# Performance work log

Measured on AMD Instinct MI355X. Metric: run time of the kernel, lower is better.

Reference implementation:

```python
import jax, jax.numpy as jnp
import numpy as np

B, T, D = 4, 2048, 2048
H = 16
HO = D // H  # head_out = 128


def setup_inputs() -> dict:
    key = jax.random.key(0)
    ks = jax.random.split(key, 6)
    x = jax.random.normal(ks[0], (B, T, D), dtype=jnp.float32)
    scale = 0.02
    Wq = jax.random.normal(ks[1], (D, D), dtype=jnp.float32) * scale
    Wk = jax.random.normal(ks[2], (D, D), dtype=jnp.float32) * scale
    Wv = jax.random.normal(ks[3], (D, D), dtype=jnp.float32) * scale
    Wp = jax.random.normal(ks[4], (D, D), dtype=jnp.float32) * scale
    bp = jnp.zeros((D,), dtype=jnp.float32)
    return {"x": x, "Wq": Wq, "Wk": Wk, "Wv": Wv, "Wp": Wp, "bp": bp}


def reference(x, Wq, Wk, Wv, Wp, bp):
    b, t, _ = x.shape
    # QKV projections (weights stored [d_in, d_out])
    q = x @ Wq
    k = x @ Wk
    v = x @ Wv
    split = lambda a: a.reshape(b, t, H, HO).transpose(0, 2, 1, 3)  # [b,H,T,ho]
    qh, kh, vh = split(q), split(k), split(v)
    # Feature attention: contract over tokens -> [b,H,ho,ho]
    scores = jnp.einsum('bhtf,bhtg->bhfg', qh, kh) / jnp.sqrt(jnp.float32(HO))
    weights = jax.nn.softmax(scores, axis=-1)  # dropout p=0.0 (identity)
    # feature_alibi: [1/T, 1/(T-1), ..., 1], broadcast over batch/head/feature
    feat_alibi = (1.0 / jnp.arange(t, 0, -1, dtype=jnp.float32)).reshape(1, 1, t, 1)
    vh = vh + feat_alibi
    # (weights @ v^T)^T : ctx[b,h,t,f] = sum_g weights[b,h,f,g] * v[b,h,t,g]
    ctx = jnp.einsum('bhfg,bhtg->bhtf', weights, vh)
    ctx = ctx.transpose(0, 2, 1, 3).reshape(b, t, H * HO)  # [b,T,d_out]
    return ctx @ Wp + bp
```

## Files before the change

kernel.cpp:

```cpp
#include <hip/hip_runtime.h>
#include <hip/hip_bf16.h>


#define Tt 2048
#define Dd 2048
#define Mm 8192

typedef __attribute__((ext_vector_type(4))) float f32x4;
typedef __attribute__((ext_vector_type(8))) short s16x8;
static_assert(sizeof(s16x8) == 16, "frag size");

typedef const __attribute__((address_space(1))) void* gptr_t;
typedef __attribute__((address_space(3))) void* lptr_t;

__device__ __forceinline__ float bf2f(ushort u) {
    union { unsigned int i; float f; } c; c.i = ((unsigned int)u) << 16; return c.f;
}
__device__ __forceinline__ ushort f2bf(float f) {
    union { float f; unsigned int i; } c; c.f = f;
    return (ushort)((c.i + 0x7FFFu + ((c.i >> 16) & 1u)) >> 16);
}
__device__ __forceinline__ void gload16(const void* g, void* l) {
    __builtin_amdgcn_global_load_lds((gptr_t)g, (lptr_t)l, 16, 0, 0);
}
__device__ __forceinline__ s16x8 ldfrag(const char* p) { return *(const s16x8*)p; }

#define MFMA_BF16(d, a, b) \
    asm("v_mfma_f32_16x16x32_bf16 %0, %1, %2, %0" : "+v"(d) : "v"(a), "v"(b))


__global__ __launch_bounds__(256) void convx_kernel(const float* __restrict__ x,
                                                    ushort* __restrict__ xb) {
    const int idx = blockIdx.x * 256 + threadIdx.x;
    const int stride = gridDim.x * 256;
    for (int i = idx; i < Mm * Dd / 4; i += stride) {
        const float4 v = *(const float4*)(x + (size_t)i * 4);
        ushort4 o; o.x = f2bf(v.x); o.y = f2bf(v.y); o.z = f2bf(v.z); o.w = f2bf(v.w);
        *(ushort4*)(xb + (size_t)i * 4) = o;
    }
}

__global__ __launch_bounds__(256) void transw_kernel(const float* __restrict__ W0,
        const float* __restrict__ W1, const float* __restrict__ W2,
        const float* __restrict__ W3, ushort* __restrict__ Wt) {
    __shared__ float tile[64][65];
    const int z = blockIdx.z;
    const float* W = (z == 0) ? W0 : (z == 1) ? W1 : (z == 2) ? W2 : W3;
    ushort* dst = Wt + (size_t)z * ((size_t)Dd * Dd);
    const int n0 = blockIdx.x * 64, k0 = blockIdx.y * 64;
    const int r4 = threadIdx.x >> 6, c = threadIdx.x & 63;
#pragma unroll
    for (int i = 0; i < 16; i++) {
        const int row = i * 4 + r4;
        tile[row][c] = W[(size_t)(k0 + row) * Dd + n0 + c];
    }
    __syncthreads();
#pragma unroll
    for (int i = 0; i < 16; i++) {
        const int row = i * 4 + r4;
        dst[(size_t)(n0 + row) * Dd + k0 + c] = f2bf(tile[c][row]);
    }
}


__device__ __forceinline__ void stage_half(char* ldsRegion, const ushort* gRegion,
                                           int ld, int half, int tid) {
#pragma unroll
    for (int j = 0; j < 2; j++) {
        const int Pb = half * 16384 + j * 8192 + (tid >> 6) * 1024;
        const int P = Pb + (tid & 63) * 16;
        const int row = P >> 7;
        const int colb = (P ^ ((row & 7) << 4)) & 127;
        gload16(gRegion + (size_t)row * ld + (colb >> 1), ldsRegion + Pb);
    }
}

template <int MODE>
__global__ __launch_bounds__(512, 2) void gemm256_kernel(
        const ushort* __restrict__ A, const ushort* __restrict__ Bt,
        void* __restrict__ Cv, const float* __restrict__ bias,
        int Kdim, int lda, int ldb, int ldc,
        size_t bstride, size_t cstride) {
    extern __shared__ char lds[];

    const int tid = threadIdx.x;
    const int lane = tid & 63;
    const int w = tid >> 6;
    const int wr = w >> 2, wc = w & 3;
    const int fr = lane & 15, fq = lane >> 4;

    const int bid = blockIdx.x;
    const int wg = (bid & 7) * 32 + (bid >> 3);
    const int m0 = (wg >> 3) * 256;
    const int n0 = (wg & 7) * 256;

    const ushort* Ag = A + (size_t)m0 * lda;
    const ushort* Bg = Bt + (size_t)blockIdx.z * bstride + (size_t)n0 * ldb;
    const int NT = Kdim >> 6;

    const int aoff = wr * 16384 + fr * 128;
    const int boff = wc * 8192 + fr * 128;
    const int xo = (fr & 7) << 4;
    const int cp0 = (fq * 16) ^ xo;
    const int cp1 = (64 + fq * 16) ^ xo;

    char* buf0 = lds;
    char* buf1 = lds + 65536;
    const char* Ab0 = buf0 + aoff;
    const char* Bb0 = buf0 + 32768 + boff;
    const char* Ab1 = buf1 + aoff;
    const char* Bb1 = buf1 + 32768 + boff;

    f32x4 acc[8][4];
#pragma unroll
    for (int i = 0; i < 8; i++)
#pragma unroll
        for (int j = 0; j < 4; j++) acc[i][j] = {0.f, 0.f, 0.f, 0.f};

    s16x8 afX[4][2], afY[4][2], bf01[2][2], bf23[2][2];

    {
        stage_half(buf0,         Ag, lda, 0, tid);
        stage_half(buf0,         Ag, lda, 1, tid);
        stage_half(buf0 + 32768, Bg, ldb, 0, tid);
        stage_half(buf0 + 32768, Bg, ldb, 1, tid);
        stage_half(buf1,         Ag + 64, lda, 0, tid);
        stage_half(buf1,         Ag + 64, lda, 1, tid);
        stage_half(buf1 + 32768, Bg + 64, ldb, 0, tid);
        stage_half(buf1 + 32768, Bg + 64, ldb, 1, tid);
        __builtin_amdgcn_sched_barrier(0);
        asm volatile("s_waitcnt vmcnt(8)" ::: "memory");
        __builtin_amdgcn_s_barrier();
    }

    const int NI = NT >> 1;
    for (int j = 0; j < NI; ++j) {
        const int e = 2 * j;
        const bool sAo = (j > 0);
        const bool sE2 = (e + 2 < NT);
        const bool sO2 = (e + 3 < NT);
        const ushort* AgO  = Ag + (size_t)(e + 1) * 64;
        const ushort* AgE2 = Ag + (size_t)(e + 2) * 64;
        const ushort* BgE2 = Bg + (size_t)(e + 2) * 64;
        const ushort* BgO2 = Bg + (size_t)(e + 3) * 64;

#pragma unroll
        for (int m = 0; m < 4; m++) {
            afX[m][0] = ldfrag(Ab0 + m * 2048 + cp0);
            afX[m][1] = ldfrag(Ab0 + m * 2048 + cp1);
        }
#pragma unroll
        for (int n = 0; n < 2; n++) {
            bf01[n][0] = ldfrag(Bb0 + n * 2048 + cp0);
            bf01[n][1] = ldfrag(Bb0 + n * 2048 + cp1);
        }
        if (sAo) stage_half(buf1, AgO, lda, 0, tid);
        __builtin_amdgcn_sched_barrier(0);
        asm volatile("s_waitcnt lgkmcnt(8)" ::: "memory");
        __builtin_amdgcn_s_barrier();
        asm volatile("s_waitcnt lgkmcnt(0)" ::: "memory");
        __builtin_amdgcn_sched_barrier(0);
        __builtin_amdgcn_s_setprio(1);
#pragma unroll
        for (int k = 0; k < 2; k++)
#pragma unroll
            for (int m = 0; m < 4; m++)
#pragma unroll
                for (int n = 0; n < 2; n++) MFMA_BF16(acc[m][n], afX[m][k], bf01[n][k]);
        __builtin_amdgcn_s_setprio(0);
        __builtin_amdgcn_s_barrier();

#pragma unroll
        for (int n = 0; n < 2; n++) {
            bf23[n][0] = ldfrag(Bb0 + (n + 2) * 2048 + cp0);
            bf23[n][1] = ldfrag(Bb0 + (n + 2) * 2048 + cp1);
        }
        if (sAo) stage_half(buf1, AgO, lda, 1, tid);
        __builtin_amdgcn_sched_barrier(0);
        __builtin_amdgcn_s_barrier();
        asm volatile("s_waitcnt lgkmcnt(0)" ::: "memory");
        __builtin_amdgcn_sched_barrier(0);
        __builtin_amdgcn_s_setprio(1);
#pragma unroll
        for (int k = 0; k < 2; k++)
#pragma unroll
            for (int m = 0; m < 4; m++)
#pragma unroll
                for (int n = 0; n < 2; n++) MFMA_BF16(acc[m][n + 2], afX[m][k], bf23[n][k]);
        __builtin_amdgcn_s_setprio(0);
        __builtin_amdgcn_s_barrier();

#pragma unroll
        for (int m = 0; m < 4; m++) {
            afY[m][0] = ldfrag(Ab0 + (m + 4) * 2048 + cp0);
            afY[m][1] = ldfrag(Ab0 + (m + 4) * 2048 + cp1);
        }
        if (sE2) stage_half(buf0 + 32768, BgE2, ldb, 0, tid);
        __builtin_amdgcn_sched_barrier(0);
        __builtin_amdgcn_s_barrier();
        asm volatile("s_waitcnt lgkmcnt(0)" ::: "memory");
        __builtin_amdgcn_sched_barrier(0);
        __builtin_amdgcn_s_setprio(1);
#pragma unroll
        for (int k = 0; k < 2; k++)
#pragma unroll
            for (int m = 0; m < 4; m++)
#pragma unroll
                for (int n = 0; n < 2; n++) MFMA_BF16(acc[m + 4][n], afY[m][k], bf01[n][k]);
        __builtin_amdgcn_s_setprio(0);
        __builtin_amdgcn_s_barrier();

        if (sE2) stage_half(buf0 + 32768, BgE2, ldb, 1, tid);
        __builtin_amdgcn_sched_barrier(0);
        __builtin_amdgcn_s_setprio(1);
#pragma unroll
        for (int k = 0; k < 2; k++)
#pragma unroll
            for (int m = 0; m < 4; m++)
#pragma unroll
                for (int n = 0; n < 2; n++) MFMA_BF16(acc[m + 4][n + 2], afY[m][k], bf23[n][k]);
        __builtin_amdgcn_s_setprio(0);
        __builtin_amdgcn_sched_barrier(0);
        if (sE2) asm volatile("s_waitcnt vmcnt(4)" ::: "memory");
        else     asm volatile("s_waitcnt vmcnt(0)" ::: "memory");
        __builtin_amdgcn_s_barrier();

#pragma unroll
        for (int m = 0; m < 4; m++) {
            afX[m][0] = ldfrag(Ab1 + m * 2048 + cp0);
            afX[m][1] = ldfrag(Ab1 + m * 2048 + cp1);
        }
#pragma unroll
        for (int n = 0; n < 2; n++) {
            bf01[n][0] = ldfrag(Bb1 + n * 2048 + cp0);
            bf01[n][1] = ldfrag(Bb1 + n * 2048 + cp1);
        }
        if (sE2) stage_half(buf0, AgE2, lda, 0, tid);
        __builtin_amdgcn_sched_barrier(0);
        asm volatile("s_waitcnt lgkmcnt(8)" ::: "memory");
        __builtin_amdgcn_s_barrier();
        asm volatile("s_waitcnt lgkmcnt(0)" ::: "memory");
        __builtin_amdgcn_sched_barrier(0);
        __builtin_amdgcn_s_setprio(1);
#pragma unroll
        for (int k = 0; k < 2; k++)
#pragma unroll
            for (int m = 0; m < 4; m++)
#pragma unroll
                for (int n = 0; n < 2; n++) MFMA_BF16(acc[m][n], afX[m][k], bf01[n][k]);
        __builtin_amdgcn_s_setprio(0);
        __builtin_amdgcn_s_barrier();

#pragma unroll
        for (int n = 0; n < 2; n++) {
            bf23[n][0] = ldfrag(Bb1 + (n + 2) * 2048 + cp0);
            bf23[n][1] = ldfrag(Bb1 + (n + 2) * 2048 + cp1);
        }
        if (sE2) stage_half(buf0, AgE2, lda, 1, tid);
        __builtin_amdgcn_sched_barrier(0);
        __builtin_amdgcn_s_barrier();
        asm volatile("s_waitcnt lgkmcnt(0)" ::: "memory");
        __builtin_amdgcn_sched_barrier(0);
        __builtin_amdgcn_s_setprio(1);
#pragma unroll
        for (int k = 0; k < 2; k++)
#pragma unroll
            for (int m = 0; m < 4; m++)
#pragma unroll
                for (int n = 0; n < 2; n++) MFMA_BF16(acc[m][n + 2], afX[m][k], bf23[n][k]);
        __builtin_amdgcn_s_setprio(0);
        __builtin_amdgcn_s_barrier();

#pragma unroll
        for (int m = 0; m < 4; m++) {
            afY[m][0] = ldfrag(Ab1 + (m + 4) * 2048 + cp0);
            afY[m][1] = ldfrag(Ab1 + (m + 4) * 2048 + cp1);
        }
        if (sO2) stage_half(buf1 + 32768, BgO2, ldb, 0, tid);
        __builtin_amdgcn_sched_barrier(0);
        __builtin_amdgcn_s_barrier();
        asm volatile("s_waitcnt lgkmcnt(0)" ::: "memory");
        __builtin_amdgcn_sched_barrier(0);
        __builtin_amdgcn_s_setprio(1);
#pragma unroll
        for (int k = 0; k < 2; k++)
#pragma unroll
            for (int m = 0; m < 4; m++)
#pragma unroll
                for (int n = 0; n < 2; n++) MFMA_BF16(acc[m + 4][n], afY[m][k], bf01[n][k]);
        __builtin_amdgcn_s_setprio(0);
        __builtin_amdgcn_s_barrier();

        if (sO2) stage_half(buf1 + 32768, BgO2, ldb, 1, tid);
        __builtin_amdgcn_sched_barrier(0);
        __builtin_amdgcn_s_setprio(1);
#pragma unroll
        for (int k = 0; k < 2; k++)
#pragma unroll
            for (int m = 0; m < 4; m++)
#pragma unroll
                for (int n = 0; n < 2; n++) MFMA_BF16(acc[m + 4][n + 2], afY[m][k], bf23[n][k]);
        __builtin_amdgcn_s_setprio(0);
        __builtin_amdgcn_sched_barrier(0);
        if (sO2) asm volatile("s_waitcnt vmcnt(4)" ::: "memory");
        else     asm volatile("s_waitcnt vmcnt(0)" ::: "memory");
        __builtin_amdgcn_s_barrier();
    }

    asm volatile("s_nop 7\ns_nop 7\ns_nop 7");

    if (MODE == 2) {
        float* C = (float*)Cv;
#pragma unroll
        for (int mi = 0; mi < 8; mi++)
#pragma unroll
            for (int ni = 0; ni < 4; ni++)
#pragma unroll
                for (int r = 0; r < 4; r++) {
                    const int row = m0 + wr * 128 + mi * 16 + fq * 4 + r;
                    const int col = n0 + wc * 64 + ni * 16 + fr;
                    C[(size_t)row * ldc + col] = acc[mi][ni][r] + bias[col];
                }
    } else {
        ushort* C = (ushort*)Cv + (size_t)blockIdx.z * cstride;
#pragma unroll
        for (int mi = 0; mi < 8; mi++)
#pragma unroll
            for (int ni = 0; ni < 4; ni++)
#pragma unroll
                for (int r = 0; r < 4; r++) {
                    const int row = m0 + wr * 128 + mi * 16 + fq * 4 + r;
                    const int col = n0 + wc * 64 + ni * 16 + fr;
                    C[(size_t)row * ldc + col] = f2bf(acc[mi][ni][r]);
                }
    }
}


template <int MODE>
__global__ __launch_bounds__(256, 2) void gemm_kernel(
        const ushort* __restrict__ A, const ushort* __restrict__ Bt,
        void* __restrict__ Cv, const float* __restrict__ bias,
        int Kdim, int lda, int ldb, int ldc) {
    __shared__ ushort lsA[128 * 32];
    __shared__ ushort lsB[128 * 32];

    const int tid = threadIdx.x;
    const int w = tid >> 6, lane = tid & 63;
    const int m0 = blockIdx.y * 128;
    const int n0 = blockIdx.x * 128;

    const ushort* Ab = A;
    const ushort* Bb = Bt;
    size_t coff = 0;
    if (MODE == 1) {
        const int z = blockIdx.z, b = z >> 4, h = z & 15;
        const size_t ao = (size_t)b * ((size_t)Tt * Dd) + (size_t)h * 128;
        Ab += ao; Bb += (size_t)z * (128 * 128); coff = ao;
    }

    const int sr = lane >> 2;
    const int sc = (lane & 3) * 8;
    const int c0 = w, c1 = w + 4;
    const int rA0 = c0 * 16 + sr, rA1 = c1 * 16 + sr;

    const int fr = lane & 15, fq = lane >> 4;
    const int wr = (w >> 1) * 64, wc = (w & 1) * 64;

    f32x4 acc[4][4];
#pragma unroll
    for (int i = 0; i < 4; i++)
#pragma unroll
        for (int j = 0; j < 4; j++) acc[i][j] = {0.f, 0.f, 0.f, 0.f};

    for (int kt = 0; kt < Kdim; kt += 32) {
        gload16(Ab + (size_t)(m0 + rA0) * lda + kt + sc, lsA + c0 * 512);
        gload16(Ab + (size_t)(m0 + rA1) * lda + kt + sc, lsA + c1 * 512);
        gload16(Bb + (size_t)(n0 + rA0) * ldb + kt + sc, lsB + c0 * 512);
        gload16(Bb + (size_t)(n0 + rA1) * ldb + kt + sc, lsB + c1 * 512);
        __syncthreads();

        s16x8 afrag[4], bfrag[4];
#pragma unroll
        for (int i = 0; i < 4; i++)
            afrag[i] = *(const s16x8*)(lsA + (wr + i * 16 + fr) * 32 + fq * 8);
#pragma unroll
        for (int j = 0; j < 4; j++)
            bfrag[j] = *(const s16x8*)(lsB + (wc + j * 16 + fr) * 32 + fq * 8);
#pragma unroll
        for (int i = 0; i < 4; i++)
#pragma unroll
            for (int j = 0; j < 4; j++)
                MFMA_BF16(acc[i][j], afrag[i], bfrag[j]);
        __syncthreads();
    }

    asm volatile("s_nop 7\ns_nop 7\ns_nop 7");

    {
        ushort* C = (ushort*)Cv + coff;
#pragma unroll
        for (int i = 0; i < 4; i++)
#pragma unroll
            for (int j = 0; j < 4; j++)
#pragma unroll
                for (int r = 0; r < 4; r++) {
                    const int row = m0 + wr + i * 16 + fq * 4 + r;
                    const int col = n0 + wc + j * 16 + fr;
                    float val = acc[i][j][r];
                    if (MODE == 1) val += 1.0f / (float)(Tt - row);
                    C[(size_t)row * ldc + col] = f2bf(val);
                }
    }
}


__global__ __launch_bounds__(256) void scores_kernel(const ushort* __restrict__ q,
        const ushort* __restrict__ k, float* __restrict__ part) {
    __shared__ float lsQ[32][128];
    __shared__ float lsK[32][128];
    const int tid = threadIdx.x;
    const int s = blockIdx.x, bh = blockIdx.y;
    const int b = bh >> 4, h = bh & 15;
    const size_t base = (size_t)b * ((size_t)Tt * Dd) + (size_t)h * 128;
    const ushort* qb = q + base;
    const ushort* kb = k + base;
    const int ty = tid >> 4, tx = tid & 15;
    const int f0 = ty * 8, g0 = tx * 8;

    float acc[8][8];
#pragma unroll
    for (int i = 0; i < 8; i++)
#pragma unroll
        for (int j = 0; j < 8; j++) acc[i][j] = 0.f;

    for (int ch = 0; ch < 16; ch++) {
        const int t0 = s * 512 + ch * 32;
#pragma unroll
        for (int ii = 0; ii < 4; ii++) {
            const int e = ii * 1024 + tid * 4;
            const int r = e >> 7, cc = e & 127;
            const size_t ga = (size_t)(t0 + r) * Dd + cc;
            const ushort4 v4 = *(const ushort4*)(qb + ga);
            f32x4 qf = {bf2f(v4.x), bf2f(v4.y), bf2f(v4.z), bf2f(v4.w)};
            *(f32x4*)&lsQ[r][cc] = qf;
            const ushort4 w4 = *(const ushort4*)(kb + ga);
            f32x4 kf = {bf2f(w4.x), bf2f(w4.y), bf2f(w4.z), bf2f(w4.w)};
            *(f32x4*)&lsK[r][cc] = kf;
        }
        __syncthreads();
#pragma unroll 4
        for (int tl = 0; tl < 32; tl++) {
            float qv[8], kv[8];
            *(f32x4*)&qv[0] = *(const f32x4*)&lsQ[tl][f0];
            *(f32x4*)&qv[4] = *(const f32x4*)&lsQ[tl][f0 + 4];
            *(f32x4*)&kv[0] = *(const f32x4*)&lsK[tl][g0];
            *(f32x4*)&kv[4] = *(const f32x4*)&lsK[tl][g0 + 4];
#pragma unroll
            for (int i = 0; i < 8; i++)
#pragma unroll
                for (int j = 0; j < 8; j++)
                    acc[i][j] = fmaf(qv[i], kv[j], acc[i][j]);
        }
        __syncthreads();
    }
    float* pb = part + ((size_t)s * 64 + bh) * 16384;
#pragma unroll
    for (int i = 0; i < 8; i++) {
        f32x4 o0 = {acc[i][0], acc[i][1], acc[i][2], acc[i][3]};
        f32x4 o1 = {acc[i][4], acc[i][5], acc[i][6], acc[i][7]};
        *(f32x4*)&pb[(f0 + i) * 128 + g0] = o0;
        *(f32x4*)&pb[(f0 + i) * 128 + g0 + 4] = o1;
    }
}


__global__ __launch_bounds__(256) void softmax_kernel(const float* __restrict__ part,
                                                      ushort* __restrict__ wts) {
    const int tid = threadIdx.x;
    const int wv = tid >> 6, lane = tid & 63;
    const int row = blockIdx.x * 4 + wv;
    const float* p = part + (size_t)row * 128 + lane * 2;
    float v0 = 0.f, v1 = 0.f;
#pragma unroll
    for (int s = 0; s < 4; s++) {
        const float2 t = *(const float2*)(p + (size_t)s * 1048576);
        v0 += t.x; v1 += t.y;
    }
    const float sc = 0.088388347648318447f;
    v0 *= sc; v1 *= sc;
    float m = fmaxf(v0, v1);
#pragma unroll
    for (int off = 32; off > 0; off >>= 1) m = fmaxf(m, __shfl_xor(m, off));
    const float e0 = __expf(v0 - m), e1 = __expf(v1 - m);
    float smv = e0 + e1;
#pragma unroll
    for (int off = 32; off > 0; off >>= 1) smv += __shfl_xor(smv, off);
    const float inv = 1.0f / smv;
    ushort2 o; o.x = f2bf(e0 * inv); o.y = f2bf(e1 * inv);
    *(ushort2*)(wts + (size_t)row * 128 + lane * 2) = o;
}


extern "C" void kernel_launch(void* const* d_in, const int* in_sizes, int n_in,
                              void* d_out, int out_size, void* d_ws, size_t ws_size,
                              hipStream_t stream) {
    const float* x  = (const float*)d_in[0];
    const float* Wq = (const float*)d_in[1];
    const float* Wk = (const float*)d_in[2];
    const float* Wv = (const float*)d_in[3];
    const float* Wp = (const float*)d_in[4];
    const float* bp = (const float*)d_in[5];
    float* out = (float*)d_out;
    char* ws = (char*)d_ws;

    ushort* xb   = (ushort*)(ws);
    ushort* Wt   = (ushort*)(ws + (33ull << 20));
    ushort* q    = (ushort*)(ws + (65ull << 20));
    ushort* k    = (ushort*)(ws + (97ull << 20));
    ushort* v    = (ushort*)(ws + (129ull << 20));
    float*  part = (float*) (ws + (161ull << 20));
    ushort* wts  = (ushort*)(ws + (193ull << 20));
    ushort* ctx  = xb;

    const size_t WSZ = (size_t)Dd * Dd;
    const size_t QSTRIDE = (32ull << 20) / 2;

    static_cast<void>(hipFuncSetAttribute((const void*)gemm256_kernel<0>,
        hipFuncAttributeMaxDynamicSharedMemorySize, 131072));
    static_cast<void>(hipFuncSetAttribute((const void*)gemm256_kernel<2>,
        hipFuncAttributeMaxDynamicSharedMemorySize, 131072));

    convx_kernel<<<2048, 256, 0, stream>>>(x, xb);
    transw_kernel<<<dim3(32, 32, 4), 256, 0, stream>>>(Wq, Wk, Wv, Wp, Wt);

    gemm256_kernel<0><<<dim3(256, 1, 3), 512, 131072, stream>>>(
        xb, Wt, q, nullptr, 2048, 2048, 2048, 2048, WSZ, QSTRIDE);

    scores_kernel<<<dim3(4, 64), 256, 0, stream>>>(q, k, part);
    softmax_kernel<<<2048, 256, 0, stream>>>(part, wts);

    gemm_kernel<1><<<dim3(1, 16, 64), 256, 0, stream>>>(v, wts, ctx, nullptr, 128, 2048, 128, 2048);

    gemm256_kernel<2><<<dim3(256, 1, 1), 512, 131072, stream>>>(
        ctx, Wt + 3 * WSZ, out, bp, 2048, 2048, 2048, 2048, 0, 0);
}
```

Measured before the change: 376.8 us.

## Compute attention scores via per-batch Gram matrix X^T X instead of Q/K projections

Rewrites the scores as Wq_h^T (X^T X) Wk_h. It builds a bf16 transpose of x, forms a per-batch Gram matrix G = X^T X, multiplies by Wk, then runs a small MFMA GEMM (new mode 3) to produce split-K score partials. This replaces both the Q/K projection GEMMs and the scalar-FP32 scores kernel. Total GEMM FLOPs stay roughly the same, but the slow non-MFMA scores stage goes away. In exchange, the large-magnitude Gram and intermediate products are rounded to bf16, which can cost accuracy. It also switches MFMA from inline asm to the builtin and drops the trailing s_nop padding.

Measured after the change: 337.3 us. 1.12x faster.

```diff
diff --git a/kernel.cpp b/kernel.cpp
--- a/kernel.cpp
+++ b/kernel.cpp
@@ -26,17 +26,29 @@
 __device__ __forceinline__ s16x8 ldfrag(const char* p) { return *(const s16x8*)p; }
 
 #define MFMA_BF16(d, a, b) \
-    asm("v_mfma_f32_16x16x32_bf16 %0, %1, %2, %0" : "+v"(d) : "v"(a), "v"(b))
-
-
-__global__ __launch_bounds__(256) void convx_kernel(const float* __restrict__ x,
-                                                    ushort* __restrict__ xb) {
-    const int idx = blockIdx.x * 256 + threadIdx.x;
-    const int stride = gridDim.x * 256;
-    for (int i = idx; i < Mm * Dd / 4; i += stride) {
-        const float4 v = *(const float4*)(x + (size_t)i * 4);
-        ushort4 o; o.x = f2bf(v.x); o.y = f2bf(v.y); o.z = f2bf(v.z); o.w = f2bf(v.w);
-        *(ushort4*)(xb + (size_t)i * 4) = o;
+    d = __builtin_amdgcn_mfma_f32_16x16x32_bf16((a), (b), (d), 0, 0, 0)
+
+
+__global__ __launch_bounds__(256) void convxT_kernel(const float* __restrict__ x,
+        ushort* __restrict__ xb, ushort* __restrict__ xT) {
+    __shared__ float tile[64][65];
+    const int b = blockIdx.z;
+    const int t0 = blockIdx.y * 64, d0 = blockIdx.x * 64;
+    const int r4 = threadIdx.x >> 6, c = threadIdx.x & 63;
+#pragma unroll
+    for (int i = 0; i < 16; i++) {
+        const int row = i * 4 + r4;
+        const size_t g = ((size_t)b * Tt + t0 + row) * Dd + d0 + c;
+        const float val = x[g];
+        xb[g] = f2bf(val);
+        tile[row][c] = val;
+    }
+    __syncthreads();
+#pragma unroll
+    for (int i = 0; i < 16; i++) {
+        const int row = i * 4 + r4;
+        xT[(size_t)b * ((size_t)Dd * Tt) + (size_t)(d0 + row) * Tt + t0 + c] =
+            f2bf(tile[c][row]);
     }
 }
 
@@ -80,7 +92,7 @@
         const ushort* __restrict__ A, const ushort* __restrict__ Bt,
         void* __restrict__ Cv, const float* __restrict__ bias,
         int Kdim, int lda, int ldb, int ldc,
-        size_t bstride, size_t cstride) {
+        size_t astride, size_t bstride, size_t cstride) {
     extern __shared__ char lds[];
 
     const int tid = threadIdx.x;
@@ -90,11 +102,12 @@
     const int fr = lane & 15, fq = lane >> 4;
 
     const int bid = blockIdx.x;
-    const int wg = (bid & 7) * 32 + (bid >> 3);
+    const int cpx = (int)gridDim.x >> 3;
+    const int wg = (bid & 7) * cpx + (bid >> 3);
     const int m0 = (wg >> 3) * 256;
     const int n0 = (wg & 7) * 256;
 
-    const ushort* Ag = A + (size_t)m0 * lda;
+    const ushort* Ag = A + (size_t)blockIdx.z * astride + (size_t)m0 * lda;
     const ushort* Bg = Bt + (size_t)blockIdx.z * bstride + (size_t)n0 * ldb;
     const int NT = Kdim >> 6;
 
@@ -307,8 +320,6 @@
         __builtin_amdgcn_s_barrier();
     }
 
-    asm volatile("s_nop 7\ns_nop 7\ns_nop 7");
-
     if (MODE == 2) {
         float* C = (float*)Cv;
 #pragma unroll
@@ -358,6 +369,13 @@
         const size_t ao = (size_t)b * ((size_t)Tt * Dd) + (size_t)h * 128;
         Ab += ao; Bb += (size_t)z * (128 * 128); coff = ao;
     }
+    if (MODE == 3) {
+        const int z = blockIdx.z, s = z >> 6, bh = z & 63;
+        const int b = bh >> 4, h = bh & 15;
+        Ab += (size_t)h * 128 * Dd + (size_t)s * 512;
+        Bb += (size_t)b * ((size_t)Dd * Dd) + (size_t)h * 128 * Dd + (size_t)s * 512;
+        coff = (size_t)s * (64 * 16384) + (size_t)bh * 16384;
+    }
 
     const int sr = lane >> 2;
     const int sc = (lane & 3) * 8;
@@ -395,9 +413,19 @@
         __syncthreads();
     }
 
-    asm volatile("s_nop 7\ns_nop 7\ns_nop 7");
-
-    {
+    if (MODE == 3) {
+        float* C = (float*)Cv + coff;
+#pragma unroll
+        for (int i = 0; i < 4; i++)
+#pragma unroll
+            for (int j = 0; j < 4; j++)
+#pragma unroll
+                for (int r = 0; r < 4; r++) {
+                    const int row = m0 + wr + i * 16 + fq * 4 + r;
+                    const int col = n0 + wc + j * 16 + fr;
+                    C[(size_t)row * ldc + col] = acc[i][j][r];
+                }
+    } else {
         ushort* C = (ushort*)Cv + coff;
 #pragma unroll
         for (int i = 0; i < 4; i++)
@@ -411,66 +439,6 @@
                     if (MODE == 1) val += 1.0f / (float)(Tt - row);
                     C[(size_t)row * ldc + col] = f2bf(val);
                 }
-    }
-}
-
-
-__global__ __launch_bounds__(256) void scores_kernel(const ushort* __restrict__ q,
-        const ushort* __restrict__ k, float* __restrict__ part) {
-    __shared__ float lsQ[32][128];
-    __shared__ float lsK[32][128];
-    const int tid = threadIdx.x;
-    const int s = blockIdx.x, bh = blockIdx.y;
-    const int b = bh >> 4, h = bh & 15;
-    const size_t base = (size_t)b * ((size_t)Tt * Dd) + (size_t)h * 128;
-    const ushort* qb = q + base;
-    const ushort* kb = k + base;
-    const int ty = tid >> 4, tx = tid & 15;
-    const int f0 = ty * 8, g0 = tx * 8;
-
-    float acc[8][8];
-#pragma unroll
-    for (int i = 0; i < 8; i++)
-#pragma unroll
-        for (int j = 0; j < 8; j++) acc[i][j] = 0.f;
-
-    for (int ch = 0; ch < 16; ch++) {
-        const int t0 = s * 512 + ch * 32;
-#pragma unroll
-        for (int ii = 0; ii < 4; ii++) {
-            const int e = ii * 1024 + tid * 4;
-            const int r = e >> 7, cc = e & 127;
-            const size_t ga = (size_t)(t0 + r) * Dd + cc;
-            const ushort4 v4 = *(const ushort4*)(qb + ga);
-            f32x4 qf = {bf2f(v4.x), bf2f(v4.y), bf2f(v4.z), bf2f(v4.w)};
-            *(f32x4*)&lsQ[r][cc] = qf;
-            const ushort4 w4 = *(const ushort4*)(kb + ga);
-            f32x4 kf = {bf2f(w4.x), bf2f(w4.y), bf2f(w4.z), bf2f(w4.w)};
-            *(f32x4*)&lsK[r][cc] = kf;
-        }
-        __syncthreads();
-#pragma unroll 4
-        for (int tl = 0; tl < 32; tl++) {
-            float qv[8], kv[8];
-            *(f32x4*)&qv[0] = *(const f32x4*)&lsQ[tl][f0];
-            *(f32x4*)&qv[4] = *(const f32x4*)&lsQ[tl][f0 + 4];
-            *(f32x4*)&kv[0] = *(const f32x4*)&lsK[tl][g0];
-            *(f32x4*)&kv[4] = *(const f32x4*)&lsK[tl][g0 + 4];
-#pragma unroll
-            for (int i = 0; i < 8; i++)
-#pragma unroll
-                for (int j = 0; j < 8; j++)
-                    acc[i][j] = fmaf(qv[i], kv[j], acc[i][j]);
-        }
-        __syncthreads();
-    }
-    float* pb = part + ((size_t)s * 64 + bh) * 16384;
-#pragma unroll
-    for (int i = 0; i < 8; i++) {
-        f32x4 o0 = {acc[i][0], acc[i][1], acc[i][2], acc[i][3]};
-        f32x4 o1 = {acc[i][4], acc[i][5], acc[i][6], acc[i][7]};
-        *(f32x4*)&pb[(f0 + i) * 128 + g0] = o0;
-        *(f32x4*)&pb[(f0 + i) * 128 + g0 + 4] = o1;
     }
 }
 
@@ -514,34 +482,43 @@
     float* out = (float*)d_out;
     char* ws = (char*)d_ws;
 
-    ushort* xb   = (ushort*)(ws);
-    ushort* Wt   = (ushort*)(ws + (33ull << 20));
-    ushort* q    = (ushort*)(ws + (65ull << 20));
-    ushort* k    = (ushort*)(ws + (97ull << 20));
-    ushort* v    = (ushort*)(ws + (129ull << 20));
-    float*  part = (float*) (ws + (161ull << 20));
-    ushort* wts  = (ushort*)(ws + (193ull << 20));
-    ushort* ctx  = xb;
+    ushort* xb  = (ushort*)(ws);
+    ushort* xT  = (ushort*)(ws + (32ull << 20));
+    ushort* Wt  = (ushort*)(ws + (64ull << 20));
+    ushort* G   = (ushort*)(ws + (96ull << 20));
+    ushort* Hb  = (ushort*)(ws + (128ull << 20));
+    ushort* v   = (ushort*)(ws + (160ull << 20));
+    float*  part = (float*)(ws + (96ull << 20));
+    ushort* wts = (ushort*)(ws + (112ull << 20));
+    ushort* ctx = xT;
 
     const size_t WSZ = (size_t)Dd * Dd;
-    const size_t QSTRIDE = (32ull << 20) / 2;
 
     static_cast<void>(hipFuncSetAttribute((const void*)gemm256_kernel<0>,
         hipFuncAttributeMaxDynamicSharedMemorySize, 131072));
     static_cast<void>(hipFuncSetAttribute((const void*)gemm256_kernel<2>,
         hipFuncAttributeMaxDynamicSharedMemorySize, 131072));
 
-    convx_kernel<<<2048, 256, 0, stream>>>(x, xb);
+    convxT_kernel<<<dim3(32, 32, 4), 256, 0, stream>>>(x, xb, xT);
     transw_kernel<<<dim3(32, 32, 4), 256, 0, stream>>>(Wq, Wk, Wv, Wp, Wt);
 
-    gemm256_kernel<0><<<dim3(256, 1, 3), 512, 131072, stream>>>(
-        xb, Wt, q, nullptr, 2048, 2048, 2048, 2048, WSZ, QSTRIDE);
-
-    scores_kernel<<<dim3(4, 64), 256, 0, stream>>>(q, k, part);
+    gemm256_kernel<0><<<dim3(64, 1, 4), 512, 131072, stream>>>(
+        xT, xT, G, nullptr, 2048, 2048, 2048, 2048, WSZ, WSZ, WSZ);
+
+    gemm256_kernel<0><<<dim3(64, 1, 4), 512, 131072, stream>>>(
+        Wt + WSZ, G, Hb, nullptr, 2048, 2048, 2048, 2048, 0, WSZ, WSZ);
+
+    gemm256_kernel<0><<<dim3(256, 1, 1), 512, 131072, stream>>>(
+        xb, Wt + 2 * WSZ, v, nullptr, 2048, 2048, 2048, 2048, 0, 0, 0);
+
+    gemm_kernel<3><<<dim3(1, 1, 256), 256, 0, stream>>>(
+        Wt, Hb, part, nullptr, 512, 2048, 2048, 128);
+
     softmax_kernel<<<2048, 256, 0, stream>>>(part, wts);
 
-    gemm_kernel<1><<<dim3(1, 16, 64), 256, 0, stream>>>(v, wts, ctx, nullptr, 128, 2048, 128, 2048);
+    gemm_kernel<1><<<dim3(1, 16, 64), 256, 0, stream>>>(
+        v, wts, ctx, nullptr, 128, 2048, 128, 2048);
 
     gemm256_kernel<2><<<dim3(256, 1, 1), 512, 131072, stream>>>(
-        ctx, Wt + 3 * WSZ, out, bp, 2048, 2048, 2048, 2048, 0, 0);
-}
+        ctx, Wt + 3 * WSZ, out, bp, 2048, 2048, 2048, 2048, 0, 0, 0);
+}
```
